# Optimization experiments

Measured on AMD Instinct MI355X. Metric: run time of the kernel, lower is better.

## Reference

```python
import jax, jax.numpy as jnp
import numpy as np

N = 100000   # nodes
E = 25000    # hyperedges
M = 640000   # incidence pairs
D = 128      # feature dim (in == out, so no res_linear)
EPS = 1e-5


def setup_inputs() -> dict:
    key = jax.random.key(0)
    ks = jax.random.split(key, 7)
    X = jax.random.normal(ks[0], (N, D), dtype=jnp.float32)
    X0 = jax.random.normal(ks[1], (N, D), dtype=jnp.float32)
    vertex = jax.random.randint(ks[2], (M,), 0, N)
    edges = jax.random.randint(ks[3], (M,), 0, E)
    degE = jax.random.uniform(ks[4], (E, 1), dtype=jnp.float32)
    degV = jax.random.uniform(ks[5], (N, 1), dtype=jnp.float32)
    # xavier-uniform-ish linear weight, no bias
    W = jax.random.normal(ks[6], (D, D), dtype=jnp.float32) * np.float32(1.0 / np.sqrt(D))
    ln_w = jnp.ones((D,), dtype=jnp.float32)
    ln_b = jnp.zeros((D,), dtype=jnp.float32)
    alpha = jnp.asarray(0.1, dtype=jnp.float32)
    beta = jnp.asarray(0.5, dtype=jnp.float32)
    return {"X": X, "X0": X0, "degE": degE, "degV": degV, "W": W,
            "alpha": alpha, "beta": beta, "ln_w": ln_w, "ln_b": ln_b,
            "vertex": vertex, "edges": edges}


def reference(X, X0, degE, degV, W, alpha, beta, ln_w, ln_b, vertex, edges):
    # vertex -> hyperedge aggregation (mean), then degree scale
    Xve = X[vertex]                                          # [M, D]
    esum = jax.ops.segment_sum(Xve, edges, num_segments=E)   # [E, D]
    ecnt = jax.ops.segment_sum(jnp.ones((Xve.shape[0], 1), X.dtype), edges, num_segments=E)
    Xe = (esum / jnp.maximum(ecnt, 1.0)) * degE              # [E, D]
    # hyperedge -> vertex aggregation (sum), degree scale
    Xev = Xe[edges]                                          # [M, D]
    Xv = jax.ops.segment_sum(Xev, vertex, num_segments=N) * degV  # [N, D]
    # residual: in_features == out_features -> residual = Xv itself
    Xh = Xv + Xv
    # LayerNorm over feature dim
    mu = jnp.mean(Xh, axis=-1, keepdims=True)
    var = jnp.mean((Xh - mu) ** 2, axis=-1, keepdims=True)
    Xn = (Xh - mu) * jax.lax.rsqrt(var + EPS) * ln_w + ln_b
    # GCNII combination
    Xi = (1.0 - alpha) * Xn + alpha * X0
    return (1.0 - beta) * Xi + beta * (Xi @ W.T)
```

## Files before the change

### kernel.cpp

```cpp
#include <hip/hip_runtime.h>
#include <hip/hip_fp16.h>
#include <hip/hip_bf16.h>

#define D 128
#define NRR 16
#define NCH 32
#define CVT_BLOCKS 512
#define RE_SL 1600
#define RV_SL 6272

typedef __attribute__((ext_vector_type(8))) short bf16x8;
typedef __attribute__((ext_vector_type(4))) float f32x4;

__device__ __forceinline__ __half2 u2h(unsigned u) { return __builtin_bit_cast(__half2, u); }

__global__ __launch_bounds__(512) void count_tab(
    const int* __restrict__ edges, const int* __restrict__ vertex,
    int* __restrict__ T_E, int* __restrict__ T_V, int E, int N, int M,
    const float* __restrict__ X, uint2* __restrict__ Xh, int xn4) {
  __shared__ int he[RE_SL];
  __shared__ int hv[RV_SL];
  int b = blockIdx.x;
  if (b >= NRR * NCH) {
    const f32x4* X4 = (const f32x4*)X;
    int stride = (gridDim.x - NRR * NCH) * 512;
    for (int i = (b - NRR * NCH) * 512 + threadIdx.x; i < xn4; i += stride) {
      f32x4 v = X4[i];
      __half2 h0 = __float22half2_rn(make_float2(v[0], v[1]));
      __half2 h1 = __float22half2_rn(make_float2(v[2], v[3]));
      Xh[i] = make_uint2(__builtin_bit_cast(unsigned, h0), __builtin_bit_cast(unsigned, h1));
    }
    return;
  }
  int r = b & (NRR - 1), c = b >> 4;
  int RE = (E + NRR - 1) / NRR, RV = (N + NRR - 1) / NRR;
  int eLo = r * RE, eHi = min(eLo + RE, E);
  int vLo = r * RV, vHi = min(vLo + RV, N);
  int eLen = eHi - eLo, vLen = vHi - vLo;
  for (int i = threadIdx.x; i < eLen; i += 512) he[i] = 0;
  for (int i = threadIdx.x; i < vLen; i += 512) hv[i] = 0;
  __syncthreads();
  int m4 = M >> 2;
  int per = (m4 + NCH - 1) / NCH;
  int i0 = c * per, i1 = min(i0 + per, m4);
  for (int i = i0 + threadIdx.x; i < i1; i += 512) {
    int4 ek = ((const int4*)edges)[i];
    int4 vk = ((const int4*)vertex)[i];
    if (ek.x >= eLo && ek.x < eHi) atomicAdd(&he[ek.x - eLo], 1);
    if (ek.y >= eLo && ek.y < eHi) atomicAdd(&he[ek.y - eLo], 1);
    if (ek.z >= eLo && ek.z < eHi) atomicAdd(&he[ek.z - eLo], 1);
    if (ek.w >= eLo && ek.w < eHi) atomicAdd(&he[ek.w - eLo], 1);
    if (vk.x >= vLo && vk.x < vHi) atomicAdd(&hv[vk.x - vLo], 1);
    if (vk.y >= vLo && vk.y < vHi) atomicAdd(&hv[vk.y - vLo], 1);
    if (vk.z >= vLo && vk.z < vHi) atomicAdd(&hv[vk.z - vLo], 1);
    if (vk.w >= vLo && vk.w < vHi) atomicAdd(&hv[vk.w - vLo], 1);
  }
  if (c == NCH - 1) {
    for (int m = (m4 << 2) + threadIdx.x; m < M; m += 512) {
      int e = edges[m], v = vertex[m];
      if (e >= eLo && e < eHi) atomicAdd(&he[e - eLo], 1);
      if (v >= vLo && v < vHi) atomicAdd(&hv[v - vLo], 1);
    }
  }
  __syncthreads();
  for (int i = threadIdx.x; i < eLen; i += 512) T_E[(size_t)c * E + eLo + i] = he[i];
  for (int i = threadIdx.x; i < vLen; i += 512) T_V[(size_t)c * N + vLo + i] = hv[i];
}

__global__ __launch_bounds__(256) void chunk_prefix(
    int* __restrict__ T_E, int* __restrict__ C_E, int E,
    int* __restrict__ T_V, int* __restrict__ C_V, int N) {
  int stride = gridDim.x * 256;
  int total = E + N;
  for (int i = blockIdx.x * 256 + threadIdx.x; i < total; i += stride) {
    if (i < E) {
      int run = 0;
      #pragma unroll
      for (int c = 0; c < NCH; ++c) {
        int t = T_E[(size_t)c * E + i];
        T_E[(size_t)c * E + i] = run;
        run += t;
      }
      C_E[i] = run;
    } else {
      int id = i - E;
      int run = 0;
      #pragma unroll
      for (int c = 0; c < NCH; ++c) {
        int t = T_V[(size_t)c * N + id];
        T_V[(size_t)c * N + id] = run;
        run += t;
      }
      C_V[id] = run;
    }
  }
}

__device__ __forceinline__ int block_exscan(int x, int tid, int* wsum) {
  int lane = tid & 63, w = tid >> 6;
  int v = x;
  #pragma unroll
  for (int off = 1; off < 64; off <<= 1) {
    int t = __shfl_up(v, off);
    if (lane >= off) v += t;
  }
  if (lane == 63) wsum[w] = v;
  __syncthreads();
  if (w == 0 && lane < 16) {
    int s = wsum[lane];
    #pragma unroll
    for (int off = 1; off < 16; off <<= 1) {
      int t = __shfl_up(s, off);
      if (lane >= off) s += t;
    }
    wsum[lane] = s;
  }
  __syncthreads();
  int woff = (w == 0) ? 0 : wsum[w - 1];
  return woff + v - x;
}

__global__ __launch_bounds__(1024) void scan_local(
    const int* __restrict__ C_E, int* __restrict__ A_E, int lenE,
    const int* __restrict__ C_V, int* __restrict__ A_V, int lenN,
    int* __restrict__ sums, int BE) {
  __shared__ int wsum[16];
  int b = blockIdx.x;
  const int* C = (b < BE) ? C_E : C_V;
  int* A = (b < BE) ? A_E : A_V;
  int len = (b < BE) ? lenE : lenN;
  int base = ((b < BE) ? b : (b - BE)) << 10;
  int i = base + threadIdx.x;
  int x = (i < len) ? C[i] : 0;
  int ex = block_exscan(x, threadIdx.x, wsum);
  if (i < len) A[i] = ex;
  if (threadIdx.x == 0) sums[b] = wsum[15];
}

__global__ __launch_bounds__(1024) void scan_sums(int* __restrict__ sums, int BE, int BV) {
  __shared__ int wsum[16];
  int off = (blockIdx.x == 0) ? 0 : BE;
  int len = (blockIdx.x == 0) ? BE : BV;
  int x = (threadIdx.x < len) ? sums[off + threadIdx.x] : 0;
  int ex = block_exscan(x, threadIdx.x, wsum);
  if (threadIdx.x < len) sums[off + threadIdx.x] = ex;
}

__global__ __launch_bounds__(1024) void scan_add(
    int* __restrict__ A_E, int lenE, int* __restrict__ A_V, int lenN,
    const int* __restrict__ sums, int BE) {
  int b = blockIdx.x;
  int* A = (b < BE) ? A_E : A_V;
  int len = (b < BE) ? lenE : lenN;
  int base = ((b < BE) ? b : (b - BE)) << 10;
  int i = base + threadIdx.x;
  if (i < len) A[i] += sums[b];
}

__global__ __launch_bounds__(512) void scatter_tab(
    const int* __restrict__ edges, const int* __restrict__ vertex,
    const int* __restrict__ A_E, const int* __restrict__ A_V,
    const int* __restrict__ T_E, const int* __restrict__ T_V,
    int* __restrict__ colE, int* __restrict__ colV, int E, int N, int M) {
  __shared__ int offE[RE_SL];
  __shared__ int curE[RE_SL];
  __shared__ int offV[RV_SL];
  __shared__ int curV[RV_SL];
  int b = blockIdx.x;
  int r = b & (NRR - 1), c = b >> 4;
  int RE = (E + NRR - 1) / NRR, RV = (N + NRR - 1) / NRR;
  int eLo = r * RE, eHi = min(eLo + RE, E);
  int vLo = r * RV, vHi = min(vLo + RV, N);
  int eLen = eHi - eLo, vLen = vHi - vLo;
  for (int i = threadIdx.x; i < eLen; i += 512) {
    offE[i] = A_E[eLo + i] + T_E[(size_t)c * E + eLo + i];
    curE[i] = 0;
  }
  for (int i = threadIdx.x; i < vLen; i += 512) {
    offV[i] = A_V[vLo + i] + T_V[(size_t)c * N + vLo + i];
    curV[i] = 0;
  }
  __syncthreads();
  int m4 = M >> 2;
  int per = (m4 + NCH - 1) / NCH;
  int i0 = c * per, i1 = min(i0 + per, m4);
  for (int i = i0 + threadIdx.x; i < i1; i += 512) {
    int4 ek = ((const int4*)edges)[i];
    int4 vk = ((const int4*)vertex)[i];
    int es[4] = {ek.x, ek.y, ek.z, ek.w};
    int vs[4] = {vk.x, vk.y, vk.z, vk.w};
    #pragma unroll
    for (int t = 0; t < 4; ++t) {
      if (es[t] >= eLo && es[t] < eHi) {
        int p = atomicAdd(&curE[es[t] - eLo], 1);
        colE[offE[es[t] - eLo] + p] = vs[t];
      }
      if (vs[t] >= vLo && vs[t] < vHi) {
        int p = atomicAdd(&curV[vs[t] - vLo], 1);
        colV[offV[vs[t] - vLo] + p] = es[t];
      }
    }
  }
  if (c == NCH - 1) {
    for (int m = (m4 << 2) + threadIdx.x; m < M; m += 512) {
      int e = edges[m], v = vertex[m];
      if (e >= eLo && e < eHi) {
        int p = atomicAdd(&curE[e - eLo], 1);
        colE[offE[e - eLo] + p] = v;
      }
      if (v >= vLo && v < vHi) {
        int p = atomicAdd(&curV[v - vLo], 1);
        colV[offV[v - vLo] + p] = e;
      }
    }
  }
}

__global__ __launch_bounds__(256) void edge_agg_h2(
    const uint2* __restrict__ Xh, const float* __restrict__ degE,
    const int* __restrict__ A_E, const int* __restrict__ C_E,
    const int* __restrict__ colE, uint2* __restrict__ Xe_h, int E) {
  int eid = blockIdx.x * 4 + (threadIdx.x >> 6);
  int lane = threadIdx.x & 63;
  if (eid >= E) return;
  int s = A_E[eid], cnt = C_E[eid], e = s + cnt;
  int half = lane >> 5, fl = lane & 31;
  __half2 accA = u2h(0u), accB = u2h(0u);
  int idx = s;
  for (; idx + 8 <= e; idx += 8) {
    int ra = colE[idx + 0 + half];
    int rb = colE[idx + 2 + half];
    int rc = colE[idx + 4 + half];
    int rd = colE[idx + 6 + half];
    uint2 va = Xh[(size_t)ra * 32 + fl];
    uint2 vb = Xh[(size_t)rb * 32 + fl];
    uint2 vc = Xh[(size_t)rc * 32 + fl];
    uint2 vd = Xh[(size_t)rd * 32 + fl];
    accA = __hadd2(accA, __hadd2(__hadd2(u2h(va.x), u2h(vb.x)), __hadd2(u2h(vc.x), u2h(vd.x))));
    accB = __hadd2(accB, __hadd2(__hadd2(u2h(va.y), u2h(vb.y)), __hadd2(u2h(vc.y), u2h(vd.y))));
  }
  int rem = e - idx;
  if (rem > 0) {
    int r[4];
    #pragma unroll
    for (int t = 0; t < 4; ++t) {
      int p = 2 * t + half;
      r[t] = colE[idx + (p < rem ? p : 0)];
    }
    #pragma unroll
    for (int t = 0; t < 4; ++t) {
      uint2 v = Xh[(size_t)r[t] * 32 + fl];
      if (2 * t + half < rem) {
        accA = __hadd2(accA, u2h(v.x));
        accB = __hadd2(accB, u2h(v.y));
      }
    }
  }
  float2 fA = __half22float2(accA), fB = __half22float2(accB);
  float t0 = fA.x, t1 = fA.y, t2 = fB.x, t3 = fB.y;
  t0 += __shfl_xor(t0, 32);
  t1 += __shfl_xor(t1, 32);
  t2 += __shfl_xor(t2, 32);
  t3 += __shfl_xor(t3, 32);
  if (lane < 32) {
    float scale = degE[eid] / fmaxf((float)cnt, 1.0f);
    __half2 h0 = __float22half2_rn(make_float2(t0 * scale, t1 * scale));
    __half2 h1 = __float22half2_rn(make_float2(t2 * scale, t3 * scale));
    Xe_h[(size_t)eid * 32 + fl] =
        make_uint2(__builtin_bit_cast(unsigned, h0), __builtin_bit_cast(unsigned, h1));
  }
}

__global__ __launch_bounds__(256) void vertex_ln_h(
    const uint2* __restrict__ Xe_h, const float* __restrict__ X0,
    const float* __restrict__ degV, const float* __restrict__ ln_w,
    const float* __restrict__ ln_b, const float* __restrict__ alpha_p,
    const int* __restrict__ A_V, const int* __restrict__ C_V,
    const int* __restrict__ colV, ushort* __restrict__ Xi_bf, int N) {
  int fl = threadIdx.x & 31;
  int n = blockIdx.x * 8 + (threadIdx.x >> 5);
  if (n >= N) return;
  int s = A_V[n], cnt = C_V[n];
  __half2 accA = u2h(0u), accB = u2h(0u);
  int idx = s, rem = cnt;
  while (rem > 0) {
    int r[8];
    #pragma unroll
    for (int t = 0; t < 8; ++t) r[t] = colV[idx + (t < rem ? t : 0)];
    #pragma unroll
    for (int t = 0; t < 8; ++t) {
      uint2 v = Xe_h[(size_t)r[t] * 32 + fl];
      if (t < rem) {
        accA = __hadd2(accA, u2h(v.x));
        accB = __hadd2(accB, u2h(v.y));
      }
    }
    idx += 8;
    rem -= 8;
  }
  float2 fA = __half22float2(accA), fB = __half22float2(accB);
  float t0 = fA.x, t1 = fA.y, t2 = fB.x, t3 = fB.y;
  float sm = (t0 + t1) + (t2 + t3);
  float q = t0 * t0 + t1 * t1 + t2 * t2 + t3 * t3;
  #pragma unroll
  for (int off = 1; off < 32; off <<= 1) {
    sm += __shfl_xor(sm, off);
    q += __shfl_xor(q, off);
  }
  float dv = degV[n];
  float csc = 2.f * dv;
  float mu = csc * sm * (1.f / 128.f);
  float var = csc * csc * q * (1.f / 128.f) - mu * mu;
  float rstd = rsqrtf(var + 1e-5f);
  f32x4 lw = ((const f32x4*)ln_w)[fl];
  f32x4 lb = ((const f32x4*)ln_b)[fl];
  f32x4 x0 = ((const f32x4*)X0)[(size_t)n * 32 + fl];
  float alpha = *alpha_p;
  float tt[4] = {t0, t1, t2, t3};
  ushort ob[4];
  #pragma unroll
  for (int i = 0; i < 4; ++i) {
    float xh = csc * tt[i];
    float xn = (xh - mu) * rstd * lw[i] + lb[i];
    float xi = (1.f - alpha) * xn + alpha * x0[i];
    __hip_bfloat16 bb = __float2bfloat16(xi);
    ob[i] = __builtin_bit_cast(ushort, bb);
  }
  unsigned u0 = (unsigned)ob[0] | ((unsigned)ob[1] << 16);
  unsigned u1 = (unsigned)ob[2] | ((unsigned)ob[3] << 16);
  ((uint2*)Xi_bf)[(size_t)n * 32 + fl] = make_uint2(u0, u1);
}

__global__ void wprep_kernel(const float* __restrict__ W, const float* __restrict__ beta_p,
                             ushort* __restrict__ Wbf) {
  int idx = blockIdx.x * 256 + threadIdx.x;
  int j = idx >> 7, k = idx & 127;
  float beta = *beta_p;
  float v = beta * W[idx] + ((j == k) ? (1.f - beta) : 0.f);
  __hip_bfloat16 b = __float2bfloat16(v);
  Wbf[idx] = *(ushort*)&b;
}

__global__ __launch_bounds__(256) void gemm_out(
    const ushort* __restrict__ Xi_bf, const ushort* __restrict__ Wbf,
    float* __restrict__ out, int N) {
  __shared__ __align__(16) ushort Wl[128 * 128];
  for (int t = threadIdx.x; t < 2048; t += 256) {
    int j = t >> 4, chunk = t & 15;
    bf16x8 v = ((const bf16x8*)Wbf)[t];
    ((bf16x8*)Wl)[j * 16 + (chunk ^ (j & 7))] = v;
  }
  __syncthreads();
  int wv = threadIdx.x >> 6, lane = threadIdx.x & 63;
  int row0 = blockIdx.x * 128 + wv * 32;
  f32x4 acc[2][8] = {};
  #pragma unroll
  for (int ks = 0; ks < 4; ++ks) {
    bf16x8 a[2];
    #pragma unroll
    for (int rt = 0; rt < 2; ++rt) {
      int row = row0 + rt * 16 + (lane & 15);
      row = row < N ? row : N - 1;
      a[rt] = *(const bf16x8*)(Xi_bf + (size_t)row * 128 + ks * 32 + (lane >> 4) * 8);
    }
    int chunk = ks * 4 + (lane >> 4);
    #pragma unroll
    for (int c = 0; c < 8; ++c) {
      int col = c * 16 + (lane & 15);
      bf16x8 bb = ((const bf16x8*)Wl)[col * 16 + (chunk ^ (col & 7))];
      acc[0][c] = __builtin_amdgcn_mfma_f32_16x16x32_bf16(a[0], bb, acc[0][c], 0, 0, 0);
      acc[1][c] = __builtin_amdgcn_mfma_f32_16x16x32_bf16(a[1], bb, acc[1][c], 0, 0, 0);
    }
  }
  #pragma unroll
  for (int rt = 0; rt < 2; ++rt) {
    #pragma unroll
    for (int c = 0; c < 8; ++c) {
      #pragma unroll
      for (int i = 0; i < 4; ++i) {
        int row = row0 + rt * 16 + (lane >> 4) * 4 + i;
        int col = c * 16 + (lane & 15);
        if (row < N) out[(size_t)row * 128 + col] = acc[rt][c][i];
      }
    }
  }
}

extern "C" void kernel_launch(void* const* d_in, const int* in_sizes, int n_in,
                              void* d_out, int out_size, void* d_ws, size_t ws_size,
                              hipStream_t stream) {
  const float* X     = (const float*)d_in[0];
  const float* X0    = (const float*)d_in[1];
  const float* degE  = (const float*)d_in[2];
  const float* degV  = (const float*)d_in[3];
  const float* W     = (const float*)d_in[4];
  const float* alpha = (const float*)d_in[5];
  const float* beta  = (const float*)d_in[6];
  const float* lnw   = (const float*)d_in[7];
  const float* lnb   = (const float*)d_in[8];
  const int* vertex  = (const int*)d_in[9];
  const int* edges   = (const int*)d_in[10];

  const int N = in_sizes[0] / D;
  const int E = in_sizes[2];
  const int M = in_sizes[9];

  const int BE = (E + 1023) >> 10;
  const int BV = (N + 1023) >> 10;

  char* p = (char*)d_ws;
  auto alloc = [&](size_t bytes) { char* r = p; p += (bytes + 255) & ~255ull; return r; };
  int* A_E  = (int*)alloc((size_t)E * 4);
  int* A_V  = (int*)alloc((size_t)N * 4);
  int* C_E  = (int*)alloc((size_t)E * 4);
  int* C_V  = (int*)alloc((size_t)N * 4);
  int* sums = (int*)alloc(1024);
  int* colE = (int*)alloc((size_t)M * 4);
  int* colV = (int*)alloc((size_t)M * 4);
  int* T_E  = (int*)alloc((size_t)NCH * E * 4);
  int* T_V  = (int*)alloc((size_t)NCH * N * 4);
  uint2* X_h  = (uint2*)alloc((size_t)N * D * 2);
  uint2* Xe_h = (uint2*)alloc((size_t)E * D * 2);
  ushort* Wbf = (ushort*)alloc(16384 * 2);
  ushort* Xi_bf = (ushort*)X_h;

  count_tab<<<NRR * NCH + CVT_BLOCKS, 512, 0, stream>>>(
      edges, vertex, T_E, T_V, E, N, M, X, X_h, N * D / 4);
  chunk_prefix<<<512, 256, 0, stream>>>(T_E, C_E, E, T_V, C_V, N);
  scan_local<<<BE + BV, 1024, 0, stream>>>(C_E, A_E, E, C_V, A_V, N, sums, BE);
  scan_sums<<<2, 1024, 0, stream>>>(sums, BE, BV);
  scan_add<<<BE + BV, 1024, 0, stream>>>(A_E, E, A_V, N, sums, BE);
  scatter_tab<<<NRR * NCH, 512, 0, stream>>>(edges, vertex, A_E, A_V, T_E, T_V,
                                             colE, colV, E, N, M);
  edge_agg_h2<<<(E + 3) / 4, 256, 0, stream>>>(X_h, degE, A_E, C_E, colE, Xe_h, E);
  vertex_ln_h<<<(N + 7) / 8, 256, 0, stream>>>(Xe_h, X0, degV, lnw, lnb, alpha,
                                               A_V, C_V, colV, Xi_bf, N);
  wprep_kernel<<<64, 256, 0, stream>>>(W, beta, Wbf);
  gemm_out<<<(N + 127) / 128, 256, 0, stream>>>(Xi_bf, Wbf, (float*)d_out, N);
}
```

Measured before the change: 143.5 us.

## Use 16-lane 128-bit gathers with fp32 accumulation in edge and vertex aggregation

Edge and vertex aggregation now assign 16 lanes per row, each loading uint4 (8 halfs), instead of 32 or 64 lanes loading uint2. Edge aggregation drops the two-half split and its cross-half shuffle, and unrolls 16 index loads per batch. Accumulation changes from half2 adds to fp32 adds, which improves accuracy but costs more VALU work and registers per lane. The intent is to cut per-lane gather instruction count and raise memory-level parallelism by processing more rows per block.

After: 135.8 us. 1.06x faster.

```diff
diff --git a/kernel.cpp b/kernel.cpp
--- a/kernel.cpp
+++ b/kernel.cpp
@@ -13,6 +13,14 @@
 typedef __attribute__((ext_vector_type(4))) float f32x4;
 
 __device__ __forceinline__ __half2 u2h(unsigned u) { return __builtin_bit_cast(__half2, u); }
+__device__ __forceinline__ unsigned pack_h2(float a, float b) {
+  __half2 h = __float22half2_rn(make_float2(a, b));
+  return __builtin_bit_cast(unsigned, h);
+}
+__device__ __forceinline__ ushort f2bf(float x) {
+  __hip_bfloat16 b = __float2bfloat16(x);
+  return __builtin_bit_cast(ushort, b);
+}
 
 __global__ __launch_bounds__(512) void count_tab(
     const int* __restrict__ edges, const int* __restrict__ vertex,
@@ -26,9 +34,7 @@
     int stride = (gridDim.x - NRR * NCH) * 512;
     for (int i = (b - NRR * NCH) * 512 + threadIdx.x; i < xn4; i += stride) {
       f32x4 v = X4[i];
-      __half2 h0 = __float22half2_rn(make_float2(v[0], v[1]));
-      __half2 h1 = __float22half2_rn(make_float2(v[2], v[3]));
-      Xh[i] = make_uint2(__builtin_bit_cast(unsigned, h0), __builtin_bit_cast(unsigned, h1));
+      Xh[i] = make_uint2(pack_h2(v[0], v[1]), pack_h2(v[2], v[3]));
     }
     return;
   }
@@ -216,72 +222,55 @@
   }
 }
 
-__global__ __launch_bounds__(256) void edge_agg_h2(
-    const uint2* __restrict__ Xh, const float* __restrict__ degE,
+__global__ __launch_bounds__(256) void edge_agg_q(
+    const uint4* __restrict__ Xh4, const float* __restrict__ degE,
     const int* __restrict__ A_E, const int* __restrict__ C_E,
-    const int* __restrict__ colE, uint2* __restrict__ Xe_h, int E) {
-  int eid = blockIdx.x * 4 + (threadIdx.x >> 6);
-  int lane = threadIdx.x & 63;
+    const int* __restrict__ colE, uint4* __restrict__ Xe4, int E) {
+  int ql = threadIdx.x & 15;
+  int eid = blockIdx.x * 16 + (threadIdx.x >> 4);
   if (eid >= E) return;
-  int s = A_E[eid], cnt = C_E[eid], e = s + cnt;
-  int half = lane >> 5, fl = lane & 31;
-  __half2 accA = u2h(0u), accB = u2h(0u);
-  int idx = s;
-  for (; idx + 8 <= e; idx += 8) {
-    int ra = colE[idx + 0 + half];
-    int rb = colE[idx + 2 + half];
-    int rc = colE[idx + 4 + half];
-    int rd = colE[idx + 6 + half];
-    uint2 va = Xh[(size_t)ra * 32 + fl];
-    uint2 vb = Xh[(size_t)rb * 32 + fl];
-    uint2 vc = Xh[(size_t)rc * 32 + fl];
-    uint2 vd = Xh[(size_t)rd * 32 + fl];
-    accA = __hadd2(accA, __hadd2(__hadd2(u2h(va.x), u2h(vb.x)), __hadd2(u2h(vc.x), u2h(vd.x))));
-    accB = __hadd2(accB, __hadd2(__hadd2(u2h(va.y), u2h(vb.y)), __hadd2(u2h(vc.y), u2h(vd.y))));
-  }
-  int rem = e - idx;
-  if (rem > 0) {
-    int r[4];
-    #pragma unroll
-    for (int t = 0; t < 4; ++t) {
-      int p = 2 * t + half;
-      r[t] = colE[idx + (p < rem ? p : 0)];
-    }
-    #pragma unroll
-    for (int t = 0; t < 4; ++t) {
-      uint2 v = Xh[(size_t)r[t] * 32 + fl];
-      if (2 * t + half < rem) {
-        accA = __hadd2(accA, u2h(v.x));
-        accB = __hadd2(accB, u2h(v.y));
-      }
-    }
-  }
-  float2 fA = __half22float2(accA), fB = __half22float2(accB);
-  float t0 = fA.x, t1 = fA.y, t2 = fB.x, t3 = fB.y;
-  t0 += __shfl_xor(t0, 32);
-  t1 += __shfl_xor(t1, 32);
-  t2 += __shfl_xor(t2, 32);
-  t3 += __shfl_xor(t3, 32);
-  if (lane < 32) {
-    float scale = degE[eid] / fmaxf((float)cnt, 1.0f);
-    __half2 h0 = __float22half2_rn(make_float2(t0 * scale, t1 * scale));
-    __half2 h1 = __float22half2_rn(make_float2(t2 * scale, t3 * scale));
-    Xe_h[(size_t)eid * 32 + fl] =
-        make_uint2(__builtin_bit_cast(unsigned, h0), __builtin_bit_cast(unsigned, h1));
-  }
-}
-
-__global__ __launch_bounds__(256) void vertex_ln_h(
-    const uint2* __restrict__ Xe_h, const float* __restrict__ X0,
+  int s = A_E[eid], cnt = C_E[eid];
+  float f0 = 0.f, f1 = 0.f, f2 = 0.f, f3 = 0.f, f4 = 0.f, f5 = 0.f, f6 = 0.f, f7 = 0.f;
+  int idx = s, rem = cnt;
+  while (rem > 0) {
+    int r[16];
+    #pragma unroll
+    for (int t = 0; t < 16; ++t) r[t] = colE[idx + (t < rem ? t : 0)];
+    #pragma unroll
+    for (int t = 0; t < 16; ++t) {
+      uint4 v = Xh4[(size_t)r[t] * 16 + ql];
+      if (t < rem) {
+        float2 p0 = __half22float2(u2h(v.x));
+        float2 p1 = __half22float2(u2h(v.y));
+        float2 p2 = __half22float2(u2h(v.z));
+        float2 p3 = __half22float2(u2h(v.w));
+        f0 += p0.x; f1 += p0.y; f2 += p1.x; f3 += p1.y;
+        f4 += p2.x; f5 += p2.y; f6 += p3.x; f7 += p3.y;
+      }
+    }
+    idx += 16;
+    rem -= 16;
+  }
+  float scale = degE[eid] / fmaxf((float)cnt, 1.0f);
+  uint4 o;
+  o.x = pack_h2(f0 * scale, f1 * scale);
+  o.y = pack_h2(f2 * scale, f3 * scale);
+  o.z = pack_h2(f4 * scale, f5 * scale);
+  o.w = pack_h2(f6 * scale, f7 * scale);
+  Xe4[(size_t)eid * 16 + ql] = o;
+}
+
+__global__ __launch_bounds__(256) void vertex_ln_q(
+    const uint4* __restrict__ Xe4, const float* __restrict__ X0,
     const float* __restrict__ degV, const float* __restrict__ ln_w,
     const float* __restrict__ ln_b, const float* __restrict__ alpha_p,
     const int* __restrict__ A_V, const int* __restrict__ C_V,
-    const int* __restrict__ colV, ushort* __restrict__ Xi_bf, int N) {
-  int fl = threadIdx.x & 31;
-  int n = blockIdx.x * 8 + (threadIdx.x >> 5);
+    const int* __restrict__ colV, uint4* __restrict__ Xi4, int N) {
+  int ql = threadIdx.x & 15;
+  int n = blockIdx.x * 16 + (threadIdx.x >> 4);
   if (n >= N) return;
   int s = A_V[n], cnt = C_V[n];
-  __half2 accA = u2h(0u), accB = u2h(0u);
+  float f0 = 0.f, f1 = 0.f, f2 = 0.f, f3 = 0.f, f4 = 0.f, f5 = 0.f, f6 = 0.f, f7 = 0.f;
   int idx = s, rem = cnt;
   while (rem > 0) {
     int r[8];
@@ -289,46 +278,57 @@
     for (int t = 0; t < 8; ++t) r[t] = colV[idx + (t < rem ? t : 0)];
     #pragma unroll
     for (int t = 0; t < 8; ++t) {
-      uint2 v = Xe_h[(size_t)r[t] * 32 + fl];
+      uint4 v = Xe4[(size_t)r[t] * 16 + ql];
       if (t < rem) {
-        accA = __hadd2(accA, u2h(v.x));
-        accB = __hadd2(accB, u2h(v.y));
+        float2 p0 = __half22float2(u2h(v.x));
+        float2 p1 = __half22float2(u2h(v.y));
+        float2 p2 = __half22float2(u2h(v.z));
+        float2 p3 = __half22float2(u2h(v.w));
+        f0 += p0.x; f1 += p0.y; f2 += p1.x; f3 += p1.y;
+        f4 += p2.x; f5 += p2.y; f6 += p3.x; f7 += p3.y;
       }
     }
     idx += 8;
     rem -= 8;
   }
-  float2 fA = __half22float2(accA), fB = __half22float2(accB);
-  float t0 = fA.x, t1 = fA.y, t2 = fB.x, t3 = fB.y;
-  float sm = (t0 + t1) + (t2 + t3);
-  float q = t0 * t0 + t1 * t1 + t2 * t2 + t3 * t3;
+  float sm = ((f0 + f1) + (f2 + f3)) + ((f4 + f5) + (f6 + f7));
+  float qq = ((f0 * f0 + f1 * f1) + (f2 * f2 + f3 * f3)) +
+             ((f4 * f4 + f5 * f5) + (f6 * f6 + f7 * f7));
   #pragma unroll
-  for (int off = 1; off < 32; off <<= 1) {
+  for (int off = 1; off < 16; off <<= 1) {
     sm += __shfl_xor(sm, off);
-    q += __shfl_xor(q, off);
+    qq += __shfl_xor(qq, off);
   }
   float dv = degV[n];
   float csc = 2.f * dv;
   float mu = csc * sm * (1.f / 128.f);
-  float var = csc * csc * q * (1.f / 128.f) - mu * mu;
+  float var = csc * csc * qq * (1.f / 128.f) - mu * mu;
   float rstd = rsqrtf(var + 1e-5f);
-  f32x4 lw = ((const f32x4*)ln_w)[fl];
-  f32x4 lb = ((const f32x4*)ln_b)[fl];
-  f32x4 x0 = ((const f32x4*)X0)[(size_t)n * 32 + fl];
+  const f32x4* lw4 = (const f32x4*)ln_w;
+  const f32x4* lb4 = (const f32x4*)ln_b;
+  const f32x4* X04 = (const f32x4*)X0;
+  f32x4 lwa = lw4[ql * 2], lwb = lw4[ql * 2 + 1];
+  f32x4 lba = lb4[ql * 2], lbb = lb4[ql * 2 + 1];
+  f32x4 x0a = X04[(size_t)n * 32 + ql * 2], x0b = X04[(size_t)n * 32 + ql * 2 + 1];
   float alpha = *alpha_p;
-  float tt[4] = {t0, t1, t2, t3};
-  ushort ob[4];
+  float ff[8] = {f0, f1, f2, f3, f4, f5, f6, f7};
+  float lww[8] = {lwa[0], lwa[1], lwa[2], lwa[3], lwb[0], lwb[1], lwb[2], lwb[3]};
+  float lbb_[8] = {lba[0], lba[1], lba[2], lba[3], lbb[0], lbb[1], lbb[2], lbb[3]};
+  float x00[8] = {x0a[0], x0a[1], x0a[2], x0a[3], x0b[0], x0b[1], x0b[2], x0b[3]};
+  ushort ob[8];
   #pragma unroll
-  for (int i = 0; i < 4; ++i) {
-    float xh = csc * tt[i];
-    float xn = (xh - mu) * rstd * lw[i] + lb[i];
-    float xi = (1.f - alpha) * xn + alpha * x0[i];
-    __hip_bfloat16 bb = __float2bfloat16(xi);
-    ob[i] = __builtin_bit_cast(ushort, bb);
-  }
-  unsigned u0 = (unsigned)ob[0] | ((unsigned)ob[1] << 16);
-  unsigned u1 = (unsigned)ob[2] | ((unsigned)ob[3] << 16);
-  ((uint2*)Xi_bf)[(size_t)n * 32 + fl] = make_uint2(u0, u1);
+  for (int i = 0; i < 8; ++i) {
+    float xh = csc * ff[i];
+    float xn = (xh - mu) * rstd * lww[i] + lbb_[i];
+    float xi = (1.f - alpha) * xn + alpha * x00[i];
+    ob[i] = f2bf(xi);
+  }
+  uint4 o;
+  o.x = (unsigned)ob[0] | ((unsigned)ob[1] << 16);
+  o.y = (unsigned)ob[2] | ((unsigned)ob[3] << 16);
+  o.z = (unsigned)ob[4] | ((unsigned)ob[5] << 16);
+  o.w = (unsigned)ob[6] | ((unsigned)ob[7] << 16);
+  Xi4[(size_t)n * 16 + ql] = o;
 }
 
 __global__ void wprep_kernel(const float* __restrict__ W, const float* __restrict__ beta_p,
@@ -337,8 +337,7 @@
   int j = idx >> 7, k = idx & 127;
   float beta = *beta_p;
   float v = beta * W[idx] + ((j == k) ? (1.f - beta) : 0.f);
-  __hip_bfloat16 b = __float2bfloat16(v);
-  Wbf[idx] = *(ushort*)&b;
+  Wbf[idx] = f2bf(v);
 }
 
 __global__ __launch_bounds__(256) void gemm_out(
@@ -420,9 +419,9 @@
   int* T_E  = (int*)alloc((size_t)NCH * E * 4);
   int* T_V  = (int*)alloc((size_t)NCH * N * 4);
   uint2* X_h  = (uint2*)alloc((size_t)N * D * 2);
-  uint2* Xe_h = (uint2*)alloc((size_t)E * D * 2);
+  uint4* Xe4  = (uint4*)alloc((size_t)E * D * 2);
   ushort* Wbf = (ushort*)alloc(16384 * 2);
-  ushort* Xi_bf = (ushort*)X_h;
+  uint4* Xi4  = (uint4*)X_h;
 
   count_tab<<<NRR * NCH + CVT_BLOCKS, 512, 0, stream>>>(
       edges, vertex, T_E, T_V, E, N, M, X, X_h, N * D / 4);
@@ -432,9 +431,10 @@
   scan_add<<<BE + BV, 1024, 0, stream>>>(A_E, E, A_V, N, sums, BE);
   scatter_tab<<<NRR * NCH, 512, 0, stream>>>(edges, vertex, A_E, A_V, T_E, T_V,
                                              colE, colV, E, N, M);
-  edge_agg_h2<<<(E + 3) / 4, 256, 0, stream>>>(X_h, degE, A_E, C_E, colE, Xe_h, E);
-  vertex_ln_h<<<(N + 7) / 8, 256, 0, stream>>>(Xe_h, X0, degV, lnw, lnb, alpha,
-                                               A_V, C_V, colV, Xi_bf, N);
+  edge_agg_q<<<(E + 15) / 16, 256, 0, stream>>>((const uint4*)X_h, degE, A_E, C_E,
+                                                colE, Xe4, E);
+  vertex_ln_q<<<(N + 15) / 16, 256, 0, stream>>>(Xe4, X0, degV, lnw, lnb, alpha,
+                                                 A_V, C_V, colV, Xi4, N);
   wprep_kernel<<<64, 256, 0, stream>>>(W, beta, Wbf);
-  gemm_out<<<(N + 127) / 128, 256, 0, stream>>>(Xi_bf, Wbf, (float*)d_out, N);
-}
+  gemm_out<<<(N + 127) / 128, 256, 0, stream>>>((const ushort*)Xi4, Wbf, (float*)d_out, N);
+}
```
